# Kernel optimization log

Measured on AMD Instinct MI355X. Metric: run time of the kernel, lower is better.

## Reference

```python
import jax, jax.numpy as jnp
import numpy as np

B, S, D, H = 4, 2048, 1024, 16
HD = D // H  # head dim = 64


def setup_inputs() -> dict:
    key = jax.random.key(0)
    ks = jax.random.split(key, 10)
    std = 1.0 / np.sqrt(D)
    return {
        "Q": jax.random.normal(ks[0], (B, S, D), jnp.float32),
        "Q_lev": jax.random.normal(ks[1], (B, S, D), jnp.float32),
        "K": jax.random.normal(ks[2], (B, S, D), jnp.float32),
        "K_lev": jax.random.normal(ks[3], (B, S, D), jnp.float32),
        "V": jax.random.normal(ks[4], (B, S, D), jnp.float32),
        "V_lev": jax.random.normal(ks[5], (B, S, D), jnp.float32),
        "Wq": jax.random.normal(ks[6], (D, D), jnp.float32) * std,
        "bq": jnp.zeros((D,), jnp.float32),
        "Wk": jax.random.normal(ks[7], (D, D), jnp.float32) * std,
        "bk": jnp.zeros((D,), jnp.float32),
        "Wv": jax.random.normal(ks[8], (D, D), jnp.float32) * std,
        "bv": jnp.zeros((D,), jnp.float32),
        "Wo": jax.random.normal(ks[9], (D, D), jnp.float32) * std,
        "bo": jnp.zeros((D,), jnp.float32),
    }


def _heads(x):
    # [B,S,D] -> [B,H,S,HD]
    return x.reshape(B, S, H, HD).transpose(0, 2, 1, 3)


def reference(Q, Q_lev, K, K_lev, V, V_lev, Wq, bq, Wk, bk, Wv, bv, Wo, bo):
    q = _heads(Q @ Wq + bq + Q_lev)
    k = _heads(K @ Wk + bk + K_lev)
    v = _heads(V @ Wv + bv + V_lev)
    scores = jnp.einsum("bhqd,bhkd->bhqk", q, k) / np.sqrt(HD).astype(np.float32)
    probs = jax.nn.softmax(scores, axis=-1)  # attn_dropout rate 0 -> identity
    ctx = jnp.einsum("bhqk,bhkd->bhqd", probs, v)
    ctx = ctx.transpose(0, 2, 1, 3).reshape(B, S, D)
    return ctx @ Wo + bo  # proj_dropout rate 0 -> identity
```

## Files before the change

kernel.cpp:

```cpp
#include <hip/hip_runtime.h>
#include <hip/hip_bf16.h>

#define Bq 4
#define Sq 2048
#define Dq 1024
#define Hq 16
#define HDq 64
#define MR (Bq*Sq)

typedef __attribute__((ext_vector_type(8))) short bf16x8;
typedef __attribute__((ext_vector_type(4))) float f32x4;
typedef __attribute__((ext_vector_type(16))) float f32x16;

__device__ __forceinline__ unsigned short f2bf(float f){
  unsigned int x = __builtin_bit_cast(unsigned int, f);
  x += 0x7fffu + ((x >> 16) & 1u);
  return (unsigned short)(x >> 16);
}

#define MFMA(a,b,c)   __builtin_amdgcn_mfma_f32_16x16x32_bf16((a),(b),(c),0,0,0)
#define MFMA32(a,b,c) __builtin_amdgcn_mfma_f32_32x32x16_bf16((a),(b),(c),0,0,0)

#define SC_Q 0.18033688f

__device__ __forceinline__ void gload16(const unsigned short* g, unsigned short* l){
  __builtin_amdgcn_global_load_lds(
      (const __attribute__((address_space(1))) void*)g,
      (__attribute__((address_space(3))) void*)l, 16, 0, 0);
}

__global__ __launch_bounds__(256) void cvt_bf16x3(
    const float* __restrict__ X0, const float* __restrict__ X1, const float* __restrict__ X2,
    unsigned short* __restrict__ O0, unsigned short* __restrict__ O1, unsigned short* __restrict__ O2)
{
  const int z = blockIdx.y;
  const float* X = z==0?X0 : z==1?X1 : X2;
  unsigned short* O = z==0?O0 : z==1?O1 : O2;
  const size_t i = ((size_t)blockIdx.x*256 + threadIdx.x)*8;
  const float4 a = *(const float4*)(X+i);
  const float4 b = *(const float4*)(X+i+4);
  union { unsigned short u[8]; int4 v; } pk;
  pk.u[0]=f2bf(a.x); pk.u[1]=f2bf(a.y); pk.u[2]=f2bf(a.z); pk.u[3]=f2bf(a.w);
  pk.u[4]=f2bf(b.x); pk.u[5]=f2bf(b.y); pk.u[6]=f2bf(b.z); pk.u[7]=f2bf(b.w);
  *(int4*)(O+i) = pk.v;
}

__global__ __launch_bounds__(256) void transpose_w(
    const float* __restrict__ W0, const float* __restrict__ W1,
    const float* __restrict__ W2, const float* __restrict__ W3,
    unsigned short* __restrict__ T0, unsigned short* __restrict__ T1,
    unsigned short* __restrict__ T2, unsigned short* __restrict__ T3)
{
  __shared__ float tile[32][33];
  const int z = blockIdx.z;
  const float* W = z==0?W0 : z==1?W1 : z==2?W2 : W3;
  unsigned short* T = z==0?T0 : z==1?T1 : z==2?T2 : T3;
  const int k0 = blockIdx.x*32, n0 = blockIdx.y*32;
  const int tx = threadIdx.x & 31, ty = threadIdx.x >> 5;
  #pragma unroll
  for (int i=0;i<4;i++) tile[ty+i*8][tx] = W[(size_t)(k0+ty+i*8)*Dq + n0+tx];
  __syncthreads();
  #pragma unroll
  for (int i=0;i<4;i++) T[(size_t)(n0+ty+i*8)*Dq + k0+tx] = f2bf(tile[tx][ty+i*8]);
}

__global__ __launch_bounds__(256) void transpose_v(
    const unsigned short* __restrict__ Vb, unsigned short* __restrict__ Vo)
{
  __shared__ unsigned short t2[64][72];
  const int bh = blockIdx.y;
  const int b = bh >> 4, h = bh & 15;
  const int s0 = blockIdx.x * 64;
  const int tid = threadIdx.x;
  const int r = tid >> 3, c8 = tid & 7;
  #pragma unroll
  for (int i=0;i<2;i++){
    int s = r + i*32;
    union { int4 v; unsigned short u[8]; } uu;
    uu.v = *(const int4*)(Vb + ((size_t)b*Sq + s0 + s)*Dq + h*HDq + c8*8);
    #pragma unroll
    for (int jj=0;jj<8;jj++){
      int j = (jj + c8) & 7;
      t2[c8*8 + j][s] = uu.u[j];
    }
  }
  __syncthreads();
  #pragma unroll
  for (int i=0;i<2;i++){
    int d = r + i*32;
    *(int4*)(Vo + ((size_t)bh*HDq + d)*Sq + s0 + c8*8) = *(const int4*)&t2[d][c8*8];
  }
}

__device__ __forceinline__ void gemm_loop(const unsigned short* __restrict__ A,
    const unsigned short* __restrict__ Bt,
    int bm, int bn, unsigned short* Al, unsigned short* Bl, f32x4 acc[4][4])
{
  const int tid = threadIdx.x;
  const int lane = tid & 63, wid = tid >> 6;
  const int lr = lane & 15, lg = lane >> 4;
  const int wm = wid >> 1, wn = wid & 1;

  const int srow = wid*32 + (lane >> 3), sch = (lane & 7)*8;
  const unsigned short* As = A  + (size_t)(bm*128 + srow)*Dq + sch;
  const unsigned short* Bs = Bt + (size_t)(bn*128 + srow)*Dq + sch;
  unsigned short* Ald = Al + wid*2048;
  unsigned short* Bld = Bl + wid*2048;

  for (int k0 = 0; k0 < Dq; k0 += 64) {
    __syncthreads();
    #pragma unroll
    for (int i=0;i<4;i++){
      gload16(As + (size_t)i*8*Dq + k0, Ald + i*512);
      gload16(Bs + (size_t)i*8*Dq + k0, Bld + i*512);
    }
    asm volatile("s_waitcnt vmcnt(0)" ::: "memory");
    __syncthreads();
    #pragma unroll
    for (int kc=0;kc<2;kc++){
      bf16x8 af[4], bfr[4];
      #pragma unroll
      for (int mt=0;mt<4;mt++) af[mt]  = *(const bf16x8*)(Al + (wm*64+mt*16+lr)*64 + kc*32 + lg*8);
      #pragma unroll
      for (int nt=0;nt<4;nt++) bfr[nt] = *(const bf16x8*)(Bl + (wn*64+nt*16+lr)*64 + kc*32 + lg*8);
      #pragma unroll
      for (int mt=0;mt<4;mt++)
        #pragma unroll
        for (int nt=0;nt<4;nt++)
          acc[mt][nt] = MFMA(af[mt], bfr[nt], acc[mt][nt]);
    }
  }
}

__global__ __launch_bounds__(256) void proj_gemm(
    const unsigned short* __restrict__ Aq, const unsigned short* __restrict__ Ak, const unsigned short* __restrict__ Av,
    const float* __restrict__ Lq, const float* __restrict__ Lk, const float* __restrict__ Lv,
    const unsigned short* __restrict__ Tq, const unsigned short* __restrict__ Tk, const unsigned short* __restrict__ Tv,
    const float* __restrict__ bqp, const float* __restrict__ bkp, const float* __restrict__ bvp,
    unsigned short* __restrict__ Oq, unsigned short* __restrict__ Ok, unsigned short* __restrict__ Ov)
{
  __shared__ __align__(16) unsigned short Al[128*64];
  __shared__ __align__(16) unsigned short Bl[128*64];
  const int z = blockIdx.z;
  const unsigned short* A = z==0?Aq : z==1?Ak : Av;
  const float* Lev = z==0?Lq : z==1?Lk : Lv;
  const unsigned short* Bt = z==0?Tq : z==1?Tk : Tv;
  const float* bias = z==0?bqp : z==1?bkp : bvp;
  unsigned short* Out = z==0?Oq : z==1?Ok : Ov;
  const float scl = (z==0) ? SC_Q : 1.0f;

  f32x4 acc[4][4];
  #pragma unroll
  for (int mt=0;mt<4;mt++)
    #pragma unroll
    for (int nt=0;nt<4;nt++) acc[mt][nt] = (f32x4){0.f,0.f,0.f,0.f};

  gemm_loop(A, Bt, blockIdx.x, blockIdx.y, Al, Bl, acc);

  const int tid = threadIdx.x, lane = tid&63, wid = tid>>6;
  const int lr = lane&15, lg = lane>>4, wm = wid>>1, wn = wid&1;
  const int colb = blockIdx.y*128 + wn*64;
  float bcol[4];
  #pragma unroll
  for (int nt=0;nt<4;nt++) bcol[nt] = bias[colb + nt*16 + lr];
  #pragma unroll
  for (int mt=0;mt<4;mt++){
    int g = blockIdx.x*128 + wm*64 + mt*16 + lg*4;
    #pragma unroll
    for (int r=0;r<4;r++){
      size_t ro = (size_t)(g+r)*Dq;
      #pragma unroll
      for (int nt=0;nt<4;nt++){
        int col = colb + nt*16 + lr;
        float v = (acc[mt][nt][r] + bcol[nt] + Lev[ro + col]) * scl;
        Out[ro + col] = f2bf(v);
      }
    }
  }
}

__device__ __forceinline__ float comb_max(float x){ return fmaxf(x, __shfl_xor(x, 32, 64)); }
__device__ __forceinline__ float comb_sum(float x){ return x + __shfl_xor(x, 32, 64); }

__device__ __forceinline__ void pack_p(const f32x16& t, int hi, bf16x8& c0, bf16x8& c1){
  unsigned w[8];
  #pragma unroll
  for (int j=0;j<8;j++)
    w[j] = (unsigned)f2bf(t[2*j]) | ((unsigned)f2bf(t[2*j+1]) << 16);
  unsigned x[8];
  #pragma unroll
  for (int j=0;j<8;j++) x[j] = (unsigned)__shfl_xor((int)w[j], 32, 64);
  union { unsigned u[4]; bf16x8 v; } p0, p1;
  p0.u[0] = hi ? x[2] : w[0];
  p0.u[1] = hi ? x[3] : w[1];
  p0.u[2] = hi ? w[2] : x[0];
  p0.u[3] = hi ? w[3] : x[1];
  p1.u[0] = hi ? x[6] : w[4];
  p1.u[1] = hi ? x[7] : w[5];
  p1.u[2] = hi ? w[6] : x[4];
  p1.u[3] = hi ? w[7] : x[5];
  c0 = p0.v; c1 = p1.v;
}

__global__ __launch_bounds__(512, 4) void attn_k(
    const unsigned short* qb, const unsigned short* __restrict__ kb,
    const unsigned short* __restrict__ vt, unsigned short* cb)
{
  __shared__ unsigned short Kl[2][64*64];
  __shared__ unsigned short Vl[2][64*64];
  __shared__ float Rl[8][32];

  const int bid = blockIdx.x;
  const int swz = (bid & 7)*64 + (bid >> 3);
  const int qt = swz & 7, bh = swz >> 3;
  const int b = bh >> 4, h = bh & 15;
  const size_t base = (size_t)b*Sq*Dq + (size_t)h*HDq;

  const int tid = threadIdx.x, lane = tid & 63, wid = tid >> 6;
  const int ln31 = lane & 31, hi = lane >> 5;
  const int q0 = qt*256 + wid*32;

  bf16x8 qf[4];
  {
    const unsigned short* qp = qb + base + (size_t)(q0 + ln31)*Dq + hi*8;
    #pragma unroll
    for (int dk=0;dk<4;dk++) qf[dk] = *(const bf16x8*)(qp + dk*16);
  }

  const int kRow = tid >> 3, kCh = tid & 7;
  const unsigned short* kSrc = kb + base + (size_t)kRow*Dq + kCh*8;
  const unsigned short* vSrc = vt + ((size_t)bh*HDq + kRow)*Sq + kCh*8;
  const int wOff = kRow*64 + ((kCh ^ (kRow & 7))*8);

  int4 kreg = *(const int4*)kSrc;
  int4 vreg = *(const int4*)vSrc;
  *(int4*)&Kl[0][wOff] = kreg;
  *(int4*)&Vl[0][wOff] = vreg;

  f32x16 o0 = (f32x16)(0.0f), o1 = (f32x16)(0.0f);
  float m = -1e30f, l = 0.f;

  for (int kt = 0; kt < Sq/64; ++kt){
    __syncthreads();
    const int p = kt & 1;
    if (kt+1 < Sq/64){
      kreg = *(const int4*)(kSrc + (size_t)(kt+1)*64*Dq);
      vreg = *(const int4*)(vSrc + (kt+1)*64);
    }

    f32x16 t0 = (f32x16)(0.0f), t1 = (f32x16)(0.0f);
    __builtin_amdgcn_s_setprio(1);
    #pragma unroll
    for (int dk=0;dk<4;dk++){
      const int c = hi + dk*2;
      bf16x8 kf0 = *(const bf16x8*)&Kl[p][(ln31)*64    + ((c ^ (ln31 & 7))*8)];
      bf16x8 kf1 = *(const bf16x8*)&Kl[p][(32+ln31)*64 + ((c ^ (ln31 & 7))*8)];
      t0 = MFMA32(kf0, qf[dk], t0);
      t1 = MFMA32(kf1, qf[dk], t1);
    }
    __builtin_amdgcn_s_setprio(0);

    float tmax = t0[0];
    #pragma unroll
    for (int r=1;r<16;r++) tmax = fmaxf(tmax, t0[r]);
    #pragma unroll
    for (int r=0;r<16;r++) tmax = fmaxf(tmax, t1[r]);
    tmax = comb_max(tmax);
    if (__any(tmax > m + 8.0f)){
      float mn = fmaxf(m, tmax);
      float al = __builtin_amdgcn_exp2f(m - mn);
      m = mn;
      l *= al;
      if (hi == 0) Rl[wid][ln31] = al;
      asm volatile("" ::: "memory");
      f32x4 av[4];
      #pragma unroll
      for (int g=0; g<4; g++) av[g] = *(const f32x4*)&Rl[wid][g*8 + hi*4];
      #pragma unroll
      for (int r=0;r<16;r++){ o0[r] *= av[r>>2][r&3]; o1[r] *= av[r>>2][r&3]; }
    }
    float tsum = 0.f;
    #pragma unroll
    for (int r=0;r<16;r++){
      float a0 = __builtin_amdgcn_exp2f(t0[r] - m); t0[r] = a0; tsum += a0;
      float a1 = __builtin_amdgcn_exp2f(t1[r] - m); t1[r] = a1; tsum += a1;
    }
    l += comb_sum(tsum);

    bf16x8 pa0, pa1, pa2, pa3;
    pack_p(t0, hi, pa0, pa1);
    pack_p(t1, hi, pa2, pa3);
    __builtin_amdgcn_s_setprio(1);
    #pragma unroll
    for (int c=0;c<4;c++){
      bf16x8 pa = c==0?pa0 : c==1?pa1 : c==2?pa2 : pa3;
      const int vc = 2*c + hi;
      bf16x8 vf0 = *(const bf16x8*)&Vl[p][(ln31)*64    + ((vc ^ (ln31 & 7))*8)];
      bf16x8 vf1 = *(const bf16x8*)&Vl[p][(32+ln31)*64 + ((vc ^ (ln31 & 7))*8)];
      o0 = MFMA32(pa, vf0, o0);
      o1 = MFMA32(pa, vf1, o1);
    }
    __builtin_amdgcn_s_setprio(0);

    if (kt+1 < Sq/64){
      const int pn = p ^ 1;
      *(int4*)&Kl[pn][wOff] = kreg;
      *(int4*)&Vl[pn][wOff] = vreg;
    }
  }

  float linv = __builtin_amdgcn_rcpf(l);
  if (hi == 0) Rl[wid][ln31] = linv;
  asm volatile("" ::: "memory");
  f32x4 lv[4];
  #pragma unroll
  for (int g=0; g<4; g++) lv[g] = *(const f32x4*)&Rl[wid][g*8 + hi*4];
  #pragma unroll
  for (int r=0;r<16;r++){
    int q = (r&3) + 8*(r>>2) + 4*hi;
    size_t ro = base + (size_t)(q0 + q)*Dq;
    cb[ro + ln31]      = f2bf(o0[r] * lv[r>>2][r&3]);
    cb[ro + 32 + ln31] = f2bf(o1[r] * lv[r>>2][r&3]);
  }
}

__global__ __launch_bounds__(256) void out_gemm(
    const unsigned short* __restrict__ Ctx, const unsigned short* __restrict__ To,
    const float* __restrict__ bop, float* __restrict__ Out)
{
  __shared__ __align__(16) unsigned short Al[128*64];
  __shared__ __align__(16) unsigned short Bl[128*64];
  f32x4 acc[4][4];
  #pragma unroll
  for (int mt=0;mt<4;mt++)
    #pragma unroll
    for (int nt=0;nt<4;nt++) acc[mt][nt] = (f32x4){0.f,0.f,0.f,0.f};

  gemm_loop(Ctx, To, blockIdx.x, blockIdx.y, Al, Bl, acc);

  const int tid = threadIdx.x, lane = tid&63, wid = tid>>6;
  const int lr = lane&15, lg = lane>>4, wm = wid>>1, wn = wid&1;
  const int colb = blockIdx.y*128 + wn*64;
  float bcol[4];
  #pragma unroll
  for (int nt=0;nt<4;nt++) bcol[nt] = bop[colb + nt*16 + lr];
  #pragma unroll
  for (int mt=0;mt<4;mt++){
    int g = blockIdx.x*128 + wm*64 + mt*16 + lg*4;
    #pragma unroll
    for (int r=0;r<4;r++){
      size_t ro = (size_t)(g+r)*Dq;
      #pragma unroll
      for (int nt=0;nt<4;nt++){
        int col = colb + nt*16 + lr;
        Out[ro + col] = acc[mt][nt][r] + bcol[nt];
      }
    }
  }
}

extern "C" void kernel_launch(void* const* d_in, const int* in_sizes, int n_in,
                              void* d_out, int out_size, void* d_ws, size_t ws_size,
                              hipStream_t stream) {
  const float* Q    = (const float*)d_in[0];
  const float* Qlev = (const float*)d_in[1];
  const float* K    = (const float*)d_in[2];
  const float* Klev = (const float*)d_in[3];
  const float* V    = (const float*)d_in[4];
  const float* Vlev = (const float*)d_in[5];
  const float* Wq   = (const float*)d_in[6];
  const float* bq   = (const float*)d_in[7];
  const float* Wk   = (const float*)d_in[8];
  const float* bk   = (const float*)d_in[9];
  const float* Wv   = (const float*)d_in[10];
  const float* bv   = (const float*)d_in[11];
  const float* Wo   = (const float*)d_in[12];
  const float* bo   = (const float*)d_in[13];

  unsigned short* qbuf = (unsigned short*)d_ws;
  unsigned short* kbuf = qbuf + (size_t)MR*Dq;
  unsigned short* vbuf = kbuf + (size_t)MR*Dq;
  unsigned short* xq   = vbuf + (size_t)MR*Dq;
  unsigned short* xk   = xq   + (size_t)MR*Dq;
  unsigned short* xv   = xk   + (size_t)MR*Dq;
  unsigned short* Tq   = xv   + (size_t)MR*Dq;
  unsigned short* Tk   = Tq + (size_t)Dq*Dq;
  unsigned short* Tv   = Tk + (size_t)Dq*Dq;
  unsigned short* To   = Tv + (size_t)Dq*Dq;
  unsigned short* vtb  = xq;

  cvt_bf16x3<<<dim3(MR*Dq/(256*8), 3), 256, 0, stream>>>(Q, K, V, xq, xk, xv);
  transpose_w<<<dim3(Dq/32, Dq/32, 4), 256, 0, stream>>>(Wq,Wk,Wv,Wo, Tq,Tk,Tv,To);
  proj_gemm<<<dim3(MR/128, Dq/128, 3), 256, 0, stream>>>(
      xq,xk,xv, Qlev,Klev,Vlev, Tq,Tk,Tv, bq,bk,bv, qbuf,kbuf,vbuf);
  transpose_v<<<dim3(Sq/64, Bq*Hq), 256, 0, stream>>>(vbuf, vtb);
  attn_k<<<dim3(512), 512, 0, stream>>>(qbuf, kbuf, vtb, qbuf);
  out_gemm<<<dim3(MR/128, Dq/128), 256, 0, stream>>>(qbuf, To, bo, (float*)d_out);
}
```

Measured before the change: 288.4 us.

## Double-buffer LDS tiles in the GEMM loop to overlap loads with MFMA

The shared GEMM main loop, used by both the QKV projection and the output projection, now keeps two LDS stages. It issues the global-to-LDS loads for the next k-tile before running the MFMAs on the current one, and waits only once per iteration after compute. Before, every load completed before any compute started, so memory latency was exposed on each tile. The cost is that each kernel's LDS use doubles to 64KB, which may lower the number of resident blocks. The first stage is also synchronised without an explicit vmcnt wait, which could race.

```diff
diff --git a/kernel.cpp b/kernel.cpp
--- a/kernel.cpp
+++ b/kernel.cpp
@@ -104,32 +104,41 @@
   const int srow = wid*32 + (lane >> 3), sch = (lane & 7)*8;
   const unsigned short* As = A  + (size_t)(bm*128 + srow)*Dq + sch;
   const unsigned short* Bs = Bt + (size_t)(bn*128 + srow)*Dq + sch;
-  unsigned short* Ald = Al + wid*2048;
-  unsigned short* Bld = Bl + wid*2048;
-
+
+  #define STAGE(buf, k0) { \
+    unsigned short* Ald = Al + (buf)*8192 + wid*2048; \
+    unsigned short* Bld = Bl + (buf)*8192 + wid*2048; \
+    _Pragma("unroll") \
+    for (int i=0;i<4;i++){ \
+      gload16(As + (size_t)i*8*Dq + (k0), Ald + i*512); \
+      gload16(Bs + (size_t)i*8*Dq + (k0), Bld + i*512); \
+    } }
+
+  STAGE(0, 0);
+  __syncthreads();
+  int cur = 0;
   for (int k0 = 0; k0 < Dq; k0 += 64) {
-    __syncthreads();
-    #pragma unroll
-    for (int i=0;i<4;i++){
-      gload16(As + (size_t)i*8*Dq + k0, Ald + i*512);
-      gload16(Bs + (size_t)i*8*Dq + k0, Bld + i*512);
-    }
-    asm volatile("s_waitcnt vmcnt(0)" ::: "memory");
-    __syncthreads();
+    if (k0 + 64 < Dq) STAGE(cur^1, k0+64);
+    const unsigned short* Ac = Al + cur*8192;
+    const unsigned short* Bc = Bl + cur*8192;
     #pragma unroll
     for (int kc=0;kc<2;kc++){
       bf16x8 af[4], bfr[4];
       #pragma unroll
-      for (int mt=0;mt<4;mt++) af[mt]  = *(const bf16x8*)(Al + (wm*64+mt*16+lr)*64 + kc*32 + lg*8);
-      #pragma unroll
-      for (int nt=0;nt<4;nt++) bfr[nt] = *(const bf16x8*)(Bl + (wn*64+nt*16+lr)*64 + kc*32 + lg*8);
+      for (int mt=0;mt<4;mt++) af[mt]  = *(const bf16x8*)(Ac + (wm*64+mt*16+lr)*64 + kc*32 + lg*8);
+      #pragma unroll
+      for (int nt=0;nt<4;nt++) bfr[nt] = *(const bf16x8*)(Bc + (wn*64+nt*16+lr)*64 + kc*32 + lg*8);
       #pragma unroll
       for (int mt=0;mt<4;mt++)
         #pragma unroll
         for (int nt=0;nt<4;nt++)
           acc[mt][nt] = MFMA(af[mt], bfr[nt], acc[mt][nt]);
     }
-  }
+    asm volatile("s_waitcnt vmcnt(0)" ::: "memory");
+    __syncthreads();
+    cur ^= 1;
+  }
+  #undef STAGE
 }
 
 __global__ __launch_bounds__(256) void proj_gemm(
@@ -139,8 +148,8 @@
     const float* __restrict__ bqp, const float* __restrict__ bkp, const float* __restrict__ bvp,
     unsigned short* __restrict__ Oq, unsigned short* __restrict__ Ok, unsigned short* __restrict__ Ov)
 {
-  __shared__ __align__(16) unsigned short Al[128*64];
-  __shared__ __align__(16) unsigned short Bl[128*64];
+  __shared__ __align__(16) unsigned short Al[2*128*64];
+  __shared__ __align__(16) unsigned short Bl[2*128*64];
   const int z = blockIdx.z;
   const unsigned short* A = z==0?Aq : z==1?Ak : Av;
   const float* Lev = z==0?Lq : z==1?Lk : Lv;
@@ -328,8 +337,8 @@
     const unsigned short* __restrict__ Ctx, const unsigned short* __restrict__ To,
     const float* __restrict__ bop, float* __restrict__ Out)
 {
-  __shared__ __align__(16) unsigned short Al[128*64];
-  __shared__ __align__(16) unsigned short Bl[128*64];
+  __shared__ __align__(16) unsigned short Al[2*128*64];
+  __shared__ __align__(16) unsigned short Bl[2*128*64];
   f32x4 acc[4][4];
   #pragma unroll
   for (int mt=0;mt<4;mt++)
```

Measured after the change: 283.0 us. No clear change (-1.9%).
